# Performance work log

Hardware: AMD Instinct MI355X
Metric: run time of the kernel (lower is better)

Reference implementation:

```python
import jax, jax.numpy as jnp
import numpy as np

B, L, D, H, T = 4096, 7, 1024, 1024, 6


def setup_inputs() -> dict:
    key = jax.random.key(0)
    ks = jax.random.split(key, 20)
    s = 0.02
    inp = {
        "encoder_output": jax.random.normal(ks[0], (B, L, D), jnp.float32),
        "xes": jax.random.randint(ks[1], (B, T, 3), 0, L, jnp.int32),
        "idx": jax.random.randint(ks[2], (B,), 0, L, jnp.int32),
        "mask": jnp.ones((B, L), jnp.int32),
        # Attention params
        "Wq": jax.random.normal(ks[3], (H, H)) * s,
        "bq": jnp.zeros((H,)),
        "Wc": jax.random.normal(ks[4], (4, H, D)) * s,  # 4 context 1x1 convs stacked
        "bc": jnp.zeros((4, H)),
        "V4": jax.random.uniform(ks[5], (4, H), minval=-1.0, maxval=1.0),
        # Decoder params
        "Wi": jax.random.normal(ks[6], (H, D)) * s,  # index_linear
        "bi": jnp.zeros((H,)),
        "Wh": jax.random.normal(ks[7], (H, D)) * s,   # linear_h (no bias)
        "Wv": jax.random.normal(ks[8], (H, D)) * s,   # linear_v
        "Wsh": jax.random.normal(ks[9], (H, D)) * s,  # linears_h
        "Wsv": jax.random.normal(ks[10], (H, D)) * s, # linears_v
        "We": jax.random.normal(ks[11], (H, H)) * s,  # linear_edge
    }
    return inp


def _gather_rows(enc, i):
    # enc: [B, L, D], i: [B] -> enc[b, i[b], :]  == diagonal(index_select) in torch
    return jnp.take_along_axis(enc, i[:, None, None], axis=1)[:, 0]


def reference(encoder_output, xes, idx, mask, Wq, bq, Wc, bc, V4, Wi, bi, Wh, Wv, Wsh, Wsv, We):
    enc = encoder_output

    # --- recurrent subtree/edge accumulation over T steps (lax.scan) ---
    def step(carry, x):
        el, st = carry
        h_i, v_i, t = x  # each [B]
        h = _gather_rows(enc, h_i)  # [B, D]
        v = _gather_rows(enc, v_i)
        edge = jnp.where((t == 0)[:, None],
                         h @ Wh.T + v @ Wv.T,
                         v @ Wsv.T + h @ Wsh.T)          # [B, H]
        subtree = jnp.maximum(st, edge @ We.T)
        qt = jax.nn.relu(el + st)  # uses previous el/st, as in torch step()
        return (edge, subtree), qt

    z = jnp.zeros((B, H), enc.dtype)
    xs = (xes[:, :, 0].T, xes[:, :, 1].T, xes[:, :, 2].T)  # [T, B] each
    _, qts = jax.lax.scan(step, (z, z), xs)
    qt = qts[-1]  # last step's qt

    # --- query construction (index_linear applied and added twice, as in source) ---
    enc_idx = _gather_rows(enc, idx)           # [B, D]
    lin_idx = enc_idx @ Wi.T + bi              # [B, H]
    query = jax.nn.relu(qt + lin_idx)
    query = jax.nn.relu(query + lin_idx)

    # --- 4-way tanh attention ---
    inp = query @ Wq.T + bq                    # same input_linear for all 4 heads
    ctx = jnp.einsum('bld,khd->kbhl', enc, Wc) + bc[:, None, :, None]  # [4,B,H,L]
    att = jnp.einsum('kh,kbhl->bkl', V4, jnp.tanh(inp[None, :, :, None] + ctx))
    att = att.reshape(B, 4 * L)                # cat order: k-major, matches torch

    mask4 = jnp.tile(mask, (1, 4))
    att = jnp.where(mask4 != 0, att, -jnp.inf)
    att = 10.0 * jnp.tanh(att)
    alpha = jax.nn.softmax(att, axis=0)        # Softmax(dim=0) over batch, as in source

    # multinomial(ans, 1): per-row categorical (row-normalized), deterministic key
    skey = jax.random.key(42)
    indices = jax.random.categorical(skey, jnp.log(alpha), axis=1)[:, None]  # [B,1]
    p = jnp.take_along_axis(alpha, indices, axis=1)                           # [B,1]

    one_hot = (jnp.arange(L)[None, :] == indices).astype(mask.dtype)          # [B,L]
    mask_out = mask - one_hot
    return indices, p, mask_out
```

## Files before the change

kernel.cpp:

```cpp
#include <hip/hip_runtime.h>

#define NB 4096
#define NL 7
#define ND 1024
#define NH 1024
#define NT 6
#define NSTEP 5
#define GAP 0.02f
#define MAXF 1024

typedef __attribute__((ext_vector_type(8))) short bf16x8;
typedef __attribute__((ext_vector_type(4))) float f32x4;

__device__ __forceinline__ unsigned rotl32(unsigned x, int r) {
  return (x << r) | (x >> (32 - r));
}

__device__ __forceinline__ void threefry2x32(unsigned k0, unsigned k1,
                                             unsigned x0, unsigned x1,
                                             unsigned& o0, unsigned& o1) {
  unsigned ks2 = k0 ^ k1 ^ 0x1BD11BDAu;
#define TFR(R) { x0 += x1; x1 = rotl32(x1, (R)); x1 ^= x0; }
  x0 += k0; x1 += k1;
  TFR(13) TFR(15) TFR(26) TFR(6)
  x0 += k1; x1 += ks2 + 1u;
  TFR(17) TFR(29) TFR(16) TFR(24)
  x0 += ks2; x1 += k0 + 2u;
  TFR(13) TFR(15) TFR(26) TFR(6)
  x0 += k0; x1 += k1 + 3u;
  TFR(17) TFR(29) TFR(16) TFR(24)
  x0 += k1; x1 += ks2 + 4u;
  TFR(13) TFR(15) TFR(26) TFR(6)
  x0 += ks2; x1 += k0 + 5u;
#undef TFR
  o0 = x0; o1 = x1;
}

__device__ __forceinline__ float gumbel_for(int b, int j) {
  unsigned o0, o1;
  threefry2x32(0u, 42u, 0u, (unsigned)(b * 28 + j), o0, o1);
  unsigned bits = o0 ^ o1;
  const float TINY = 1.17549435e-38f;
  float u = __uint_as_float((bits >> 9) | 0x3f800000u) - 1.0f;
  u = fmaxf(TINY, u + TINY);
  return -logf(-logf(u));
}

__device__ __forceinline__ unsigned short f2bf(float f) {
  unsigned u = __float_as_uint(f);
  unsigned r = u + 0x7FFFu + ((u >> 16) & 1u);
  return (unsigned short)(r >> 16);
}
__device__ __forceinline__ float bf2f(unsigned short h) {
  return __uint_as_float(((unsigned)h) << 16);
}

__global__ __launch_bounds__(256) void k_split(
    const float* __restrict__ x, unsigned short* __restrict__ hi,
    unsigned short* __restrict__ lo) {
  const size_t i = ((size_t)blockIdx.x * 256 + threadIdx.x) * 4;
  float4 v = *(const float4*)(x + i);
  ushort4 h, l;
  h.x = f2bf(v.x); l.x = f2bf(v.x - bf2f(h.x));
  h.y = f2bf(v.y); l.y = f2bf(v.y - bf2f(h.y));
  h.z = f2bf(v.z); l.z = f2bf(v.z - bf2f(h.z));
  h.w = f2bf(v.w); l.w = f2bf(v.w - bf2f(h.w));
  *(ushort4*)(hi + i) = h;
  *(ushort4*)(lo + i) = l;
}

__device__ __forceinline__ void tile_compute(const float (*As)[68],
                                             const float (*Bs)[68],
                                             float acc[4][4], int tx, int ty) {
#pragma unroll
  for (int kk = 0; kk < 16; ++kk) {
    float4 a  = *(const float4*)&As[kk][ty * 4];
    float4 bb = *(const float4*)&Bs[kk][tx * 4];
    acc[0][0] += a.x * bb.x; acc[0][1] += a.x * bb.y; acc[0][2] += a.x * bb.z; acc[0][3] += a.x * bb.w;
    acc[1][0] += a.y * bb.x; acc[1][1] += a.y * bb.y; acc[1][2] += a.y * bb.z; acc[1][3] += a.y * bb.w;
    acc[2][0] += a.z * bb.x; acc[2][1] += a.z * bb.y; acc[2][2] += a.z * bb.z; acc[2][3] += a.z * bb.w;
    acc[3][0] += a.w * bb.x; acc[3][1] += a.w * bb.y; acc[3][2] += a.w * bb.z; acc[3][3] += a.w * bb.w;
  }
}

#define TILE_DECLS \
  __shared__ float As[16][68]; \
  __shared__ float Bs[16][68]; \
  float acc[4][4] = {}; \
  const int tid = threadIdx.x; \
  const int tx = tid & 15, ty = tid >> 4; \
  const int row0 = blockIdx.y * 64, col0 = blockIdx.x * 64; \
  const int lm = tid >> 2; \
  const int lk4 = (tid & 3) * 4;

#define STORE_AS(av) { As[lk4+0][lm]=(av).x; As[lk4+1][lm]=(av).y; As[lk4+2][lm]=(av).z; As[lk4+3][lm]=(av).w; }
#define STORE_BS(bv) { Bs[lk4+0][lm]=(bv).x; Bs[lk4+1][lm]=(bv).y; Bs[lk4+2][lm]=(bv).z; Bs[lk4+3][lm]=(bv).w; }

__global__ __launch_bounds__(256) void gemm_bias(
    const float* __restrict__ A, const int* __restrict__ gidx,
    const float* __restrict__ enc, const float* __restrict__ Bw,
    const float* __restrict__ bias, float* __restrict__ C) {
  TILE_DECLS
  const int r = row0 + lm;
  const float* arow = gidx ? (enc + (((size_t)r * NL + gidx[r]) << 10))
                           : (A + ((size_t)r << 10));
  const float* brow = Bw + ((size_t)(col0 + lm) << 10);
  for (int k0 = 0; k0 < ND; k0 += 16) {
    float4 av = *(const float4*)(arow + k0 + lk4);
    STORE_AS(av)
    float4 bv = *(const float4*)(brow + k0 + lk4);
    STORE_BS(bv)
    __syncthreads();
    tile_compute(As, Bs, acc, tx, ty);
    __syncthreads();
  }
#pragma unroll
  for (int i = 0; i < 4; ++i) {
    const int rr = row0 + ty * 4 + i;
    const int n0 = col0 + tx * 4;
    float4 v = make_float4(acc[i][0] + bias[n0 + 0], acc[i][1] + bias[n0 + 1],
                           acc[i][2] + bias[n0 + 2], acc[i][3] + bias[n0 + 3]);
    *(float4*)(C + ((size_t)rr << 10) + n0) = v;
  }
}

__global__ __launch_bounds__(256) void k_classify(
    const int* __restrict__ xes, int* __restrict__ cls_cnt,
    int* __restrict__ l0, int* __restrict__ l1) {
  const int r = blockIdx.x * 256 + threadIdx.x;
  if (r >= NSTEP * NB) return;
  const int b = r & (NB - 1), t = r >> 12;
  const int tt = xes[(b * NT + t) * 3 + 2];
  if (tt == 0) { int p = atomicAdd(&cls_cnt[0], 1); l0[p] = r; }
  else         { int p = atomicAdd(&cls_cnt[1], 1); l1[p] = r; }
}

__global__ __launch_bounds__(256) void g1_mfma(
    const int* __restrict__ cls_cnt, const int* __restrict__ l0,
    const int* __restrict__ l1, const int* __restrict__ xes,
    const unsigned short* __restrict__ enc_hi, const unsigned short* __restrict__ enc_lo,
    const unsigned short* __restrict__ w4hi, const unsigned short* __restrict__ w4lo,
    unsigned* __restrict__ ehilo, float* __restrict__ edge4) {
  const int n0c = cls_cnt[0], n1c = cls_cnt[1];
  const int tiles0 = (n0c + 127) >> 7, tiles1 = (n1c + 127) >> 7;
  const int bx = blockIdx.x;
  if (bx >= tiles0 + tiles1) return;
  int cls, mtile, nc;
  const int* list;
  if (bx < tiles0) { cls = 0; mtile = bx; nc = n0c; list = l0; }
  else { cls = 1; mtile = bx - tiles0; nc = n1c; list = l1; }

  __shared__ unsigned short sAhi[4096], sAlo[4096], sBhi[4096], sBlo[4096];
  const int tid = threadIdx.x;
  const int ncol0 = blockIdx.y * 128;

  const int ri = tid & 127;
  const int c0 = tid >> 7;
  const int c1 = c0 + 2;
  const int li = mtile * 128 + ri;
  const int rsrc = list[(li < nc) ? li : (nc - 1)];
  const int b = rsrc & (NB - 1), t = rsrc >> 12;
  const int hidx = xes[(b * NT + t) * 3 + 0];
  const int vidx = xes[(b * NT + t) * 3 + 1];
  const unsigned short* ha = enc_hi + (((size_t)b * NL + hidx) << 10);
  const unsigned short* la = enc_lo + (((size_t)b * NL + hidx) << 10);
  const unsigned short* hb = enc_hi + (((size_t)b * NL + vidx) << 10);
  const unsigned short* lb = enc_lo + (((size_t)b * NL + vidx) << 10);
  const size_t wrow = ((size_t)(ncol0 + ri)) << 10;

  const int wave = tid >> 6, lane = tid & 63;
  const int wm = wave >> 1, wn = wave & 1;
  const int q = lane >> 4, m16 = lane & 15;

  f32x4 acc[4][4] = {};

  for (int kt = 0; kt < 64; ++kt) {
    const int seg = (kt < 32) ? (cls * 2) : (cls * 2 + 1);
    const int kl = (kt & 31) * 32;
    const unsigned short* ah = (kt < 32) ? ha : hb;
    const unsigned short* al = (kt < 32) ? la : lb;
    bf16x8 vah0 = *(const bf16x8*)(ah + kl + c0 * 8);
    bf16x8 vah1 = *(const bf16x8*)(ah + kl + c1 * 8);
    bf16x8 val0 = *(const bf16x8*)(al + kl + c0 * 8);
    bf16x8 val1 = *(const bf16x8*)(al + kl + c1 * 8);
    const unsigned short* wh = w4hi + (((size_t)seg) << 20) + wrow + kl;
    const unsigned short* wl = w4lo + (((size_t)seg) << 20) + wrow + kl;
    bf16x8 vbh0 = *(const bf16x8*)(wh + c0 * 8);
    bf16x8 vbh1 = *(const bf16x8*)(wh + c1 * 8);
    bf16x8 vbl0 = *(const bf16x8*)(wl + c0 * 8);
    bf16x8 vbl1 = *(const bf16x8*)(wl + c1 * 8);
    *(bf16x8*)&sAhi[(c0 * 128 + ri) * 8] = vah0;
    *(bf16x8*)&sAhi[(c1 * 128 + ri) * 8] = vah1;
    *(bf16x8*)&sAlo[(c0 * 128 + ri) * 8] = val0;
    *(bf16x8*)&sAlo[(c1 * 128 + ri) * 8] = val1;
    *(bf16x8*)&sBhi[(c0 * 128 + ri) * 8] = vbh0;
    *(bf16x8*)&sBhi[(c1 * 128 + ri) * 8] = vbh1;
    *(bf16x8*)&sBlo[(c0 * 128 + ri) * 8] = vbl0;
    *(bf16x8*)&sBlo[(c1 * 128 + ri) * 8] = vbl1;
    __syncthreads();

    bf16x8 bh[4], bl[4];
#pragma unroll
    for (int tn = 0; tn < 4; ++tn) {
      const int nl = wn * 64 + tn * 16 + m16;
      bh[tn] = *(const bf16x8*)&sBhi[(q * 128 + nl) * 8];
      bl[tn] = *(const bf16x8*)&sBlo[(q * 128 + nl) * 8];
    }
#pragma unroll
    for (int tm = 0; tm < 4; ++tm) {
      const int ml = wm * 64 + tm * 16 + m16;
      bf16x8 ah8 = *(const bf16x8*)&sAhi[(q * 128 + ml) * 8];
      bf16x8 al8 = *(const bf16x8*)&sAlo[(q * 128 + ml) * 8];
#pragma unroll
      for (int tn = 0; tn < 4; ++tn) {
        acc[tm][tn] = __builtin_amdgcn_mfma_f32_16x16x32_bf16(ah8, bh[tn], acc[tm][tn], 0, 0, 0);
        acc[tm][tn] = __builtin_amdgcn_mfma_f32_16x16x32_bf16(al8, bh[tn], acc[tm][tn], 0, 0, 0);
        acc[tm][tn] = __builtin_amdgcn_mfma_f32_16x16x32_bf16(ah8, bl[tn], acc[tm][tn], 0, 0, 0);
      }
    }
    __syncthreads();
  }

#pragma unroll
  for (int tm = 0; tm < 4; ++tm) {
#pragma unroll
    for (int j = 0; j < 4; ++j) {
      const int rl = wm * 64 + tm * 16 + q * 4 + j;
      const int li2 = mtile * 128 + rl;
      if (li2 < nc) {
        const int rr = list[li2];
#pragma unroll
        for (int tn = 0; tn < 4; ++tn) {
          const int n = ncol0 + wn * 64 + tn * 16 + m16;
          const float val = acc[tm][tn][j];
          unsigned short h = f2bf(val);
          unsigned short l = f2bf(val - bf2f(h));
          ehilo[(size_t)rr * NH + n] = (unsigned)h | ((unsigned)l << 16);
          if (rr >= 4 * NB) edge4[(size_t)(rr - 4 * NB) * NH + n] = val;
        }
      }
    }
  }
}

__global__ __launch_bounds__(256) void g2_mfma(
    const unsigned* __restrict__ ehilo,
    const unsigned short* __restrict__ wehi, const unsigned short* __restrict__ welo,
    unsigned* __restrict__ st) {
  __shared__ unsigned short sAhi[4096], sAlo[4096], sBhi[4096], sBlo[4096];
  const int tid = threadIdx.x;
  const int row0 = blockIdx.x * 128;
  const int ncol0 = blockIdx.y * 128;

  const int ri = tid & 127;
  const int c0 = tid >> 7;
  const int c1 = c0 + 2;
  const size_t arow = (size_t)(row0 + ri) * NH;
  const size_t wrow = ((size_t)(ncol0 + ri)) << 10;

  const int wave = tid >> 6, lane = tid & 63;
  const int wm = wave >> 1, wn = wave & 1;
  const int q = lane >> 4, m16 = lane & 15;

  f32x4 acc[4][4] = {};

  for (int kt = 0; kt < 32; ++kt) {
    const int kl = kt * 32;
    uint4 p00 = *(const uint4*)(ehilo + arow + kl + c0 * 8);
    uint4 p01 = *(const uint4*)(ehilo + arow + kl + c0 * 8 + 4);
    uint4 p10 = *(const uint4*)(ehilo + arow + kl + c1 * 8);
    uint4 p11 = *(const uint4*)(ehilo + arow + kl + c1 * 8 + 4);
    bf16x8 ah0, al0, ah1, al1;
    {
      unsigned u[8] = {p00.x, p00.y, p00.z, p00.w, p01.x, p01.y, p01.z, p01.w};
#pragma unroll
      for (int i = 0; i < 8; ++i) { ah0[i] = (short)(u[i] & 0xffff); al0[i] = (short)(u[i] >> 16); }
      unsigned v[8] = {p10.x, p10.y, p10.z, p10.w, p11.x, p11.y, p11.z, p11.w};
#pragma unroll
      for (int i = 0; i < 8; ++i) { ah1[i] = (short)(v[i] & 0xffff); al1[i] = (short)(v[i] >> 16); }
    }
    bf16x8 vbh0 = *(const bf16x8*)(wehi + wrow + kl + c0 * 8);
    bf16x8 vbh1 = *(const bf16x8*)(wehi + wrow + kl + c1 * 8);
    bf16x8 vbl0 = *(const bf16x8*)(welo + wrow + kl + c0 * 8);
    bf16x8 vbl1 = *(const bf16x8*)(welo + wrow + kl + c1 * 8);
    *(bf16x8*)&sAhi[(c0 * 128 + ri) * 8] = ah0;
    *(bf16x8*)&sAhi[(c1 * 128 + ri) * 8] = ah1;
    *(bf16x8*)&sAlo[(c0 * 128 + ri) * 8] = al0;
    *(bf16x8*)&sAlo[(c1 * 128 + ri) * 8] = al1;
    *(bf16x8*)&sBhi[(c0 * 128 + ri) * 8] = vbh0;
    *(bf16x8*)&sBhi[(c1 * 128 + ri) * 8] = vbh1;
    *(bf16x8*)&sBlo[(c0 * 128 + ri) * 8] = vbl0;
    *(bf16x8*)&sBlo[(c1 * 128 + ri) * 8] = vbl1;
    __syncthreads();

    bf16x8 bh[4], bl[4];
#pragma unroll
    for (int tn = 0; tn < 4; ++tn) {
      const int nl = wn * 64 + tn * 16 + m16;
      bh[tn] = *(const bf16x8*)&sBhi[(q * 128 + nl) * 8];
      bl[tn] = *(const bf16x8*)&sBlo[(q * 128 + nl) * 8];
    }
#pragma unroll
    for (int tm = 0; tm < 4; ++tm) {
      const int ml = wm * 64 + tm * 16 + m16;
      bf16x8 ah8 = *(const bf16x8*)&sAhi[(q * 128 + ml) * 8];
      bf16x8 al8 = *(const bf16x8*)&sAlo[(q * 128 + ml) * 8];
#pragma unroll
      for (int tn = 0; tn < 4; ++tn) {
        acc[tm][tn] = __builtin_amdgcn_mfma_f32_16x16x32_bf16(ah8, bh[tn], acc[tm][tn], 0, 0, 0);
        acc[tm][tn] = __builtin_amdgcn_mfma_f32_16x16x32_bf16(al8, bh[tn], acc[tm][tn], 0, 0, 0);
        acc[tm][tn] = __builtin_amdgcn_mfma_f32_16x16x32_bf16(ah8, bl[tn], acc[tm][tn], 0, 0, 0);
      }
    }
    __syncthreads();
  }

#pragma unroll
  for (int tm = 0; tm < 4; ++tm) {
#pragma unroll
    for (int j = 0; j < 4; ++j) {
      const int rr = row0 + wm * 64 + tm * 16 + q * 4 + j;
      const int b = rr & (NB - 1);
#pragma unroll
      for (int tn = 0; tn < 4; ++tn) {
        const int n = ncol0 + wn * 64 + tn * 16 + m16;
        unsigned val = __float_as_uint(fmaxf(acc[tm][tn][j], 0.f));
        atomicMax(&st[(size_t)b * NH + n], val);
      }
    }
  }
}

__global__ __launch_bounds__(256) void g5_mfma(
    const unsigned short* __restrict__ Ahi, const unsigned short* __restrict__ Alo,
    const unsigned short* __restrict__ Bhi, const unsigned short* __restrict__ Blo,
    const float* __restrict__ inp, const float* __restrict__ bc,
    const float* __restrict__ V4, float* __restrict__ att) {
  __shared__ unsigned short sAhi[4096], sAlo[4096], sBhi[4096], sBlo[4096];
  __shared__ float red[128][32];

  const int tid = threadIdx.x;
  const int row0 = blockIdx.x * 128;
  const int ncol0 = blockIdx.y * 128;

  const int s0 = tid, s1 = tid + 256;
  const int c0 = s0 >> 7, r0 = s0 & 127;
  const int c1 = s1 >> 7, r1 = s1 & 127;
  size_t aoff0 = (size_t)(row0 + r0) * ND + c0 * 8;
  size_t aoff1 = (size_t)(row0 + r1) * ND + c1 * 8;
  size_t boff0 = (size_t)(ncol0 + r0) * ND + c0 * 8;
  size_t boff1 = (size_t)(ncol0 + r1) * ND + c1 * 8;

  const int wave = tid >> 6, lane = tid & 63;
  const int wm = wave >> 1, wn = wave & 1;
  const int q = lane >> 4, m16 = lane & 15;

  f32x4 acc[4][4] = {};

  for (int kt = 0; kt < 32; ++kt) {
    bf16x8 vah0 = *(const bf16x8*)(Ahi + aoff0);
    bf16x8 vah1 = *(const bf16x8*)(Ahi + aoff1);
    bf16x8 val0 = *(const bf16x8*)(Alo + aoff0);
    bf16x8 val1 = *(const bf16x8*)(Alo + aoff1);
    bf16x8 vbh0 = *(const bf16x8*)(Bhi + boff0);
    bf16x8 vbh1 = *(const bf16x8*)(Bhi + boff1);
    bf16x8 vbl0 = *(const bf16x8*)(Blo + boff0);
    bf16x8 vbl1 = *(const bf16x8*)(Blo + boff1);
    *(bf16x8*)&sAhi[s0 * 8] = vah0;
    *(bf16x8*)&sAhi[s1 * 8] = vah1;
    *(bf16x8*)&sAlo[s0 * 8] = val0;
    *(bf16x8*)&sAlo[s1 * 8] = val1;
    *(bf16x8*)&sBhi[s0 * 8] = vbh0;
    *(bf16x8*)&sBhi[s1 * 8] = vbh1;
    *(bf16x8*)&sBlo[s0 * 8] = vbl0;
    *(bf16x8*)&sBlo[s1 * 8] = vbl1;
    __syncthreads();

    bf16x8 bh[4], bl[4];
#pragma unroll
    for (int tn = 0; tn < 4; ++tn) {
      const int nl = wn * 64 + tn * 16 + m16;
      bh[tn] = *(const bf16x8*)&sBhi[(q * 128 + nl) * 8];
      bl[tn] = *(const bf16x8*)&sBlo[(q * 128 + nl) * 8];
    }
#pragma unroll
    for (int tm = 0; tm < 4; ++tm) {
      const int ml = wm * 64 + tm * 16 + m16;
      bf16x8 ah = *(const bf16x8*)&sAhi[(q * 128 + ml) * 8];
      bf16x8 al = *(const bf16x8*)&sAlo[(q * 128 + ml) * 8];
#pragma unroll
      for (int tn = 0; tn < 4; ++tn) {
        acc[tm][tn] = __builtin_amdgcn_mfma_f32_16x16x32_bf16(ah, bh[tn], acc[tm][tn], 0, 0, 0);
        acc[tm][tn] = __builtin_amdgcn_mfma_f32_16x16x32_bf16(al, bh[tn], acc[tm][tn], 0, 0, 0);
        acc[tm][tn] = __builtin_amdgcn_mfma_f32_16x16x32_bf16(ah, bl[tn], acc[tm][tn], 0, 0, 0);
      }
    }
    __syncthreads();
    aoff0 += 32; aoff1 += 32; boff0 += 32; boff1 += 32;
  }

  const int kq = ncol0 >> 10;
  float rowsum[16];
#pragma unroll
  for (int i = 0; i < 16; ++i) rowsum[i] = 0.f;
#pragma unroll
  for (int tm = 0; tm < 4; ++tm) {
#pragma unroll
    for (int tn = 0; tn < 4; ++tn) {
      const int n = ncol0 + wn * 64 + tn * 16 + m16;
      const int h = n & (NH - 1);
      const float v4 = V4[kq * NH + h];
      const float bcv = bc[kq * NH + h];
#pragma unroll
      for (int j = 0; j < 4; ++j) {
        const int R = row0 + wm * 64 + tm * 16 + q * 4 + j;
        const int b = R / NL;
        float val = acc[tm][tn][j] + inp[(size_t)b * NH + h] + bcv;
        rowsum[tm * 4 + j] += v4 * tanhf(val);
      }
    }
  }
#pragma unroll
  for (int tm = 0; tm < 4; ++tm)
#pragma unroll
    for (int j = 0; j < 4; ++j)
      red[wm * 64 + tm * 16 + q * 4 + j][wn * 16 + m16] = rowsum[tm * 4 + j];
  __syncthreads();
  if (tid < 128) {
    float ssum = 0.f;
#pragma unroll
    for (int x = 0; x < 32; ++x) ssum += red[tid][x];
    const int R = row0 + tid;
    const int b = R / NL, l = R - b * NL;
    atomicAdd(&att[b * 28 + kq * NL + l], ssum);
  }
}

__global__ __launch_bounds__(256) void k_query(
    const float* __restrict__ edge4, const float* __restrict__ st,
    const float* __restrict__ lin, float* __restrict__ query) {
  const size_t i = (size_t)blockIdx.x * 256 + threadIdx.x;
  float e4 = edge4[i];
  float qt = fmaxf(e4 + st[i], 0.f);
  float l = lin[i];
  float q = fmaxf(qt + l, 0.f);
  q = fmaxf(q + l, 0.f);
  query[i] = q;
}

__global__ __launch_bounds__(256) void k_finish(
    float* __restrict__ att, const int* __restrict__ mask) {
  const int i = blockIdx.x * 256 + threadIdx.x;
  const int b = i / 28;
  const int j = i - b * 28;
  const int l = j % NL;
  float v = att[i];
  att[i] = (mask[b * NL + l] != 0) ? (10.f * tanhf(v)) : -10.f;
}

__global__ __launch_bounds__(256) void k_colstats(
    const float* __restrict__ att, float* __restrict__ Mv, float* __restrict__ Sv) {
  const int j = blockIdx.x;
  const int tid = threadIdx.x;
  __shared__ float sm[256];
  float m = -INFINITY;
  for (int b = tid; b < NB; b += 256) m = fmaxf(m, att[b * 28 + j]);
  sm[tid] = m;
  __syncthreads();
  for (int s = 128; s > 0; s >>= 1) {
    if (tid < s) sm[tid] = fmaxf(sm[tid], sm[tid + s]);
    __syncthreads();
  }
  const float M = sm[0];
  __syncthreads();
  float sum = 0.f;
  for (int b = tid; b < NB; b += 256) sum += expf(att[b * 28 + j] - M);
  sm[tid] = sum;
  __syncthreads();
  for (int s = 128; s > 0; s >>= 1) {
    if (tid < s) sm[tid] += sm[tid + s];
    __syncthreads();
  }
  if (tid == 0) { Mv[j] = M; Sv[j] = sm[0]; }
}

__global__ __launch_bounds__(256) void k_sample(
    const float* __restrict__ att, const float* __restrict__ Mv,
    const float* __restrict__ Sv, const int* __restrict__ mask,
    float* __restrict__ out, int* __restrict__ flag,
    int* __restrict__ cnt, int* __restrict__ list) {
  const int b = blockIdx.x * 256 + threadIdx.x;
  if (b >= NB) return;
  float best = -INFINITY, second = -INFINITY;
  int bj = 0;
  for (int j = 0; j < 28; ++j) {
    float y = (att[b * 28 + j] - Mv[j]) - logf(Sv[j]) + gumbel_for(b, j);
    if (y > best) { second = best; best = y; bj = j; }
    else if (y > second) second = y;
  }
  out[b] = (float)bj;
  out[NB + b] = expf(att[b * 28 + bj] - Mv[bj]) / Sv[bj];
  const int* mrow = mask + b * NL;
#pragma unroll
  for (int l = 0; l < NL; ++l)
    out[2 * NB + (size_t)b * NL + l] = (float)(mrow[l] - ((l == bj) ? 1 : 0));
  const int f = (best - second < GAP) ? 1 : 0;
  flag[b] = f;
  if (f) {
    int pos = atomicAdd(cnt, 1);
    if (pos < MAXF) list[pos] = b;
  }
}

__global__ __launch_bounds__(256) void k_build_fl(
    const int* __restrict__ cnt, const int* __restrict__ list,
    const int* __restrict__ xes, int* __restrict__ fl_cnt,
    int* __restrict__ fl0, int* __restrict__ fl1) {
  const int it = blockIdx.x * 256 + threadIdx.x;
  const int n = (cnt[0] < MAXF) ? cnt[0] : MAXF;
  if (it >= n) return;
  const int b = list[it];
#pragma unroll
  for (int t = 0; t < NSTEP; ++t) {
    const int tt = xes[(b * NT + t) * 3 + 2];
    const int e = it * 8 + t;
    if (tt == 0) { int p = atomicAdd(&fl_cnt[0], 1); fl0[p] = e; }
    else         { int p = atomicAdd(&fl_cnt[1], 1); fl1[p] = e; }
  }
}

__global__ __launch_bounds__(256) void k_fix_edge(
    const int* __restrict__ fl_cnt, const int* __restrict__ fl0,
    const int* __restrict__ fl1, const int* __restrict__ list,
    const int* __restrict__ xes, const float* __restrict__ enc,
    const float* __restrict__ Wh, const float* __restrict__ Wv,
    const float* __restrict__ Wsh, const float* __restrict__ Wsv,
    float* __restrict__ edgeF) {
  const int n0c = fl_cnt[0], n1c = fl_cnt[1];
  const int tiles0 = (n0c + 63) >> 6, tiles1 = (n1c + 63) >> 6;
  const int bx = blockIdx.x;
  if (bx >= tiles0 + tiles1) return;
  int cls, mtile, nc;
  const int* fl;
  if (bx < tiles0) { cls = 0; mtile = bx; nc = n0c; fl = fl0; }
  else { cls = 1; mtile = bx - tiles0; nc = n1c; fl = fl1; }

  __shared__ float As[16][68];
  __shared__ float Bs[16][68];
  float acc[4][4] = {};
  const int tid = threadIdx.x;
  const int tx = tid & 15, ty = tid >> 4;
  const int col0 = blockIdx.y * 64;
  const int lm = tid >> 2;
  const int lk4 = (tid & 3) * 4;

  const int li = mtile * 64 + lm;
  const int e = fl[(li < nc) ? li : (nc - 1)];
  const int it = e >> 3, t = e & 7;
  const int b = list[it];
  const int hidx = xes[(b * NT + t) * 3 + 0];
  const int vidx = xes[(b * NT + t) * 3 + 1];
  const float* arow0 = enc + (((size_t)b * NL + hidx) << 10);
  const float* arow1 = enc + (((size_t)b * NL + vidx) << 10);
  const float* W0 = (cls == 0) ? Wh : Wsh;
  const float* W1 = (cls == 0) ? Wv : Wsv;
  const float* brow0 = W0 + ((size_t)(col0 + lm) << 10);
  const float* brow1 = W1 + ((size_t)(col0 + lm) << 10);

  for (int half = 0; half < 2; ++half) {
    const float* ar = half ? arow1 : arow0;
    const float* br = half ? brow1 : brow0;
    for (int k0 = 0; k0 < ND; k0 += 16) {
      float4 av = *(const float4*)(ar + k0 + lk4);
      STORE_AS(av)
      float4 bv = *(const float4*)(br + k0 + lk4);
      STORE_BS(bv)
      __syncthreads();
      tile_compute(As, Bs, acc, tx, ty);
      __syncthreads();
    }
  }
#pragma unroll
  for (int i = 0; i < 4; ++i) {
    const int li2 = mtile * 64 + ty * 4 + i;
    if (li2 < nc) {
      const int e2 = fl[li2];
      const int it2 = e2 >> 3, t2 = e2 & 7;
      *(float4*)(edgeF + (((size_t)(it2 * 5 + t2)) << 10) + col0 + tx * 4) =
          make_float4(acc[i][0], acc[i][1], acc[i][2], acc[i][3]);
    }
  }
}

__global__ __launch_bounds__(256) void k_fix_st(
    const int* __restrict__ cnt, const float* __restrict__ edgeF,
    const float* __restrict__ We, unsigned* __restrict__ stF) {
  const int n = (cnt[0] < MAXF) ? cnt[0] : MAXF;
  const int M = n * 5;
  const int tiles = (M + 63) >> 6;
  if ((int)blockIdx.x >= tiles) return;
  __shared__ float As[16][68];
  __shared__ float Bs[16][68];
  float acc[4][4] = {};
  const int tid = threadIdx.x;
  const int tx = tid & 15, ty = tid >> 4;
  const int row0 = blockIdx.x * 64, col0 = blockIdx.y * 64;
  const int lm = tid >> 2;
  const int lk4 = (tid & 3) * 4;
  const int r = row0 + lm;
  const int rc = (r < M) ? r : (M - 1);
  const float* arow = edgeF + ((size_t)rc << 10);
  const float* brow = We + ((size_t)(col0 + lm) << 10);
  for (int k0 = 0; k0 < NH; k0 += 16) {
    float4 av = *(const float4*)(arow + k0 + lk4);
    STORE_AS(av)
    float4 bv = *(const float4*)(brow + k0 + lk4);
    STORE_BS(bv)
    __syncthreads();
    tile_compute(As, Bs, acc, tx, ty);
    __syncthreads();
  }
#pragma unroll
  for (int i = 0; i < 4; ++i) {
    const int rr = row0 + ty * 4 + i;
    if (rr < M) {
      const int it = rr / 5;
#pragma unroll
      for (int j = 0; j < 4; ++j) {
        unsigned val = __float_as_uint(fmaxf(acc[i][j], 0.f));
        atomicMax(&stF[(size_t)it * NH + col0 + tx * 4 + j], val);
      }
    }
  }
}

__global__ __launch_bounds__(256) void k_fix_query(
    const int* __restrict__ cnt, const int* __restrict__ list,
    const float* __restrict__ edgeF, const float* __restrict__ stF,
    const float* __restrict__ lin, float* __restrict__ qF) {
  const int i = blockIdx.x * 256 + threadIdx.x;
  const int it = i >> 10;
  const int n = (cnt[0] < MAXF) ? cnt[0] : MAXF;
  if (it >= n) return;
  const int nn = i & (NH - 1);
  const int b = list[it];
  float e4 = edgeF[(((size_t)(it * 5 + 4)) << 10) + nn];
  float stv = stF[(size_t)it * NH + nn];
  float qt = fmaxf(e4 + stv, 0.f);
  float lb = lin[(size_t)b * NH + nn];
  float qv = fmaxf(fmaxf(qt + lb, 0.f) + lb, 0.f);
  qF[(size_t)it * NH + nn] = qv;
}

__global__ __launch_bounds__(256) void k_fix_inp(
    const int* __restrict__ cnt, const int* __restrict__ list,
    const float* __restrict__ qF, const float* __restrict__ Wq,
    const float* __restrict__ bq, float* __restrict__ inp) {
  const int n = (cnt[0] < MAXF) ? cnt[0] : MAXF;
  const int tiles = (n + 63) >> 6;
  if ((int)blockIdx.x >= tiles) return;
  __shared__ float As[16][68];
  __shared__ float Bs[16][68];
  float acc[4][4] = {};
  const int tid = threadIdx.x;
  const int tx = tid & 15, ty = tid >> 4;
  const int row0 = blockIdx.x * 64, col0 = blockIdx.y * 64;
  const int lm = tid >> 2;
  const int lk4 = (tid & 3) * 4;
  const int r = row0 + lm;
  const int rc = (r < n) ? r : (n - 1);
  const float* arow = qF + ((size_t)rc << 10);
  const float* brow = Wq + ((size_t)(col0 + lm) << 10);
  for (int k0 = 0; k0 < NH; k0 += 16) {
    float4 av = *(const float4*)(arow + k0 + lk4);
    STORE_AS(av)
    float4 bv = *(const float4*)(brow + k0 + lk4);
    STORE_BS(bv)
    __syncthreads();
    tile_compute(As, Bs, acc, tx, ty);
    __syncthreads();
  }
#pragma unroll
  for (int i = 0; i < 4; ++i) {
    const int rr = row0 + ty * 4 + i;
    if (rr < n) {
      const int b = list[rr];
      const int n0 = col0 + tx * 4;
      float4 v = make_float4(acc[i][0] + bq[n0 + 0], acc[i][1] + bq[n0 + 1],
                             acc[i][2] + bq[n0 + 2], acc[i][3] + bq[n0 + 3]);
      *(float4*)(inp + ((size_t)b << 10) + n0) = v;
    }
  }
}

__global__ __launch_bounds__(256) void k_fixup_att(
    const int* __restrict__ cnt, const int* __restrict__ list,
    const float* __restrict__ enc, const float* __restrict__ Wc,
    const float* __restrict__ bc, const float* __restrict__ V4,
    const float* __restrict__ inp, const int* __restrict__ mask,
    float* __restrict__ att) {
  const int kq = blockIdx.x;
  const int tid = threadIdx.x;
  __shared__ float sEnc[NL][ND];
  __shared__ float sm[256];
  const int n = (cnt[0] < MAXF) ? cnt[0] : MAXF;
  for (int it = blockIdx.y; it < n; it += gridDim.y) {
    const int b = list[it];
    for (int i = tid; i < NL * 256; i += 256) {
      const int l = i >> 8, c = (i & 255) * 4;
      *(float4*)&sEnc[l][c] = *(const float4*)(enc + (((size_t)b * NL + l) << 10) + c);
    }
    __syncthreads();
    float accl[NL];
#pragma unroll
    for (int l = 0; l < NL; ++l) accl[l] = 0.f;
    for (int hp = 0; hp < 2; ++hp) {
      const int h0 = tid + hp * 512;
      const int h1 = h0 + 256;
      const float* w0 = Wc + (((size_t)kq * NH + h0) << 10);
      const float* w1 = Wc + (((size_t)kq * NH + h1) << 10);
      float d0[NL], d1[NL];
#pragma unroll
      for (int l = 0; l < NL; ++l) { d0[l] = 0.f; d1[l] = 0.f; }
      for (int k = 0; k < ND; k += 4) {
        float4 a = *(const float4*)(w0 + k);
        float4 c = *(const float4*)(w1 + k);
#pragma unroll
        for (int l = 0; l < NL; ++l) {
          float4 e = *(const float4*)&sEnc[l][k];
          d0[l] += a.x * e.x + a.y * e.y + a.z * e.z + a.w * e.w;
          d1[l] += c.x * e.x + c.y * e.y + c.z * e.z + c.w * e.w;
        }
      }
      const float i0 = inp[(size_t)b * NH + h0], i1 = inp[(size_t)b * NH + h1];
      const float b0 = bc[kq * NH + h0], b1 = bc[kq * NH + h1];
      const float v0 = V4[kq * NH + h0], v1 = V4[kq * NH + h1];
#pragma unroll
      for (int l = 0; l < NL; ++l)
        accl[l] += v0 * tanhf(d0[l] + i0 + b0) + v1 * tanhf(d1[l] + i1 + b1);
    }
    for (int l = 0; l < NL; ++l) {
      sm[tid] = accl[l];
      __syncthreads();
      for (int s = 128; s > 0; s >>= 1) {
        if (tid < s) sm[tid] += sm[tid + s];
        __syncthreads();
      }
      if (tid == 0) {
        float a = (mask[b * NL + l] != 0) ? (10.f * tanhf(sm[0])) : -10.f;
        att[b * 28 + kq * NL + l] = a;
      }
      __syncthreads();
    }
    __syncthreads();
  }
}

__global__ __launch_bounds__(256) void k_resample(
    const int* __restrict__ flag, const float* __restrict__ att,
    const float* __restrict__ Mv, const float* __restrict__ Sv,
    const int* __restrict__ mask, float* __restrict__ out) {
  const int b = blockIdx.x * 256 + threadIdx.x;
  if (b >= NB) return;
  if (!flag[b]) return;
  float best = -INFINITY;
  int bj = 0;
  for (int j = 0; j < 28; ++j) {
    float y = (att[b * 28 + j] - Mv[j]) - logf(Sv[j]) + gumbel_for(b, j);
    if (y > best) { best = y; bj = j; }
  }
  out[b] = (float)bj;
  out[NB + b] = expf(att[b * 28 + bj] - Mv[bj]) / Sv[bj];
  const int* mrow = mask + b * NL;
#pragma unroll
  for (int l = 0; l < NL; ++l)
    out[2 * NB + (size_t)b * NL + l] = (float)(mrow[l] - ((l == bj) ? 1 : 0));
}

extern "C" void kernel_launch(void* const* d_in, const int* in_sizes, int n_in,
                              void* d_out, int out_size, void* d_ws, size_t ws_size,
                              hipStream_t stream) {
  const float* enc  = (const float*)d_in[0];
  const int*   xes  = (const int*)d_in[1];
  const int*   idx  = (const int*)d_in[2];
  const int*   mask = (const int*)d_in[3];
  const float* Wq   = (const float*)d_in[4];
  const float* bq   = (const float*)d_in[5];
  const float* Wc   = (const float*)d_in[6];
  const float* bc   = (const float*)d_in[7];
  const float* V4   = (const float*)d_in[8];
  const float* Wi   = (const float*)d_in[9];
  const float* bi   = (const float*)d_in[10];
  const float* Wh   = (const float*)d_in[11];
  const float* Wv   = (const float*)d_in[12];
  const float* Wsh  = (const float*)d_in[13];
  const float* Wsv  = (const float*)d_in[14];
  const float* We   = (const float*)d_in[15];
  (void)in_sizes; (void)n_in; (void)out_size; (void)ws_size;

  char* p = (char*)d_ws;
  float* edge4 = (float*)p;                 p += (size_t)NB * NH * 4;
  unsigned* ehilo = (unsigned*)p;           p += (size_t)NSTEP * NB * NH * 4;
  float* st = (float*)p;                    p += (size_t)NB * NH * 4;
  float* lin = (float*)p;                   p += (size_t)NB * NH * 4;
  float* query = (float*)p;                 p += (size_t)NB * NH * 4;
  float* inp = (float*)p;                   p += (size_t)NB * NH * 4;
  float* att = (float*)p;                   p += (size_t)NB * 28 * 4;
  float* Mv = (float*)p;                    p += 28 * 4;
  float* Sv = (float*)p;                    p += 28 * 4;
  int* flag = (int*)p;                      p += NB * 4;
  int* cnt = (int*)p;                       p += 4 * 4;
  int* list = (int*)p;                      p += NB * 4;
  int* cls_cnt = (int*)p;                   p += 2 * 4;
  int* l0 = (int*)p;                        p += NSTEP * NB * 4;
  int* l1 = (int*)p;                        p += NSTEP * NB * 4;
  int* fl_cnt = (int*)p;                    p += 2 * 4;
  int* fl0 = (int*)p;                       p += NSTEP * MAXF * 4;
  int* fl1 = (int*)p;                       p += NSTEP * MAXF * 4;
  float* edgeF = (float*)p;                 p += (size_t)NSTEP * MAXF * NH * 4;
  float* stF = (float*)p;                   p += (size_t)MAXF * NH * 4;
  float* qF = (float*)p;                    p += (size_t)MAXF * NH * 4;
  unsigned short* enc_hi = (unsigned short*)p; p += (size_t)NB * NL * ND * 2;
  unsigned short* enc_lo = (unsigned short*)p; p += (size_t)NB * NL * ND * 2;
  unsigned short* w4hi = (unsigned short*)p;   p += (size_t)4 * NH * ND * 2;
  unsigned short* w4lo = (unsigned short*)p;   p += (size_t)4 * NH * ND * 2;
  unsigned short* wehi = (unsigned short*)p;   p += (size_t)NH * ND * 2;
  unsigned short* welo = (unsigned short*)p;   p += (size_t)NH * ND * 2;
  unsigned short* wc_hi = (unsigned short*)p;  p += (size_t)4 * NH * ND * 2;
  unsigned short* wc_lo = (unsigned short*)p;  p += (size_t)4 * NH * ND * 2;
  float* out = (float*)d_out;

  hipMemsetAsync(st, 0, (size_t)NB * NH * sizeof(float), stream);
  hipMemsetAsync(att, 0, (size_t)NB * 28 * sizeof(float), stream);
  hipMemsetAsync(cnt, 0, sizeof(int), stream);
  hipMemsetAsync(cls_cnt, 0, 2 * sizeof(int), stream);
  hipMemsetAsync(fl_cnt, 0, 2 * sizeof(int), stream);
  hipMemsetAsync(stF, 0, (size_t)MAXF * NH * sizeof(float), stream);

  dim3 blk(256);
  k_split<<<dim3((NB * NL * ND) / 1024), blk, 0, stream>>>(enc, enc_hi, enc_lo);
  k_split<<<dim3((4 * NH * ND) / 1024), blk, 0, stream>>>(Wc, wc_hi, wc_lo);
  k_split<<<dim3((NH * ND) / 1024), blk, 0, stream>>>(Wh, w4hi, w4lo);
  k_split<<<dim3((NH * ND) / 1024), blk, 0, stream>>>(Wv, w4hi + (size_t)NH * ND, w4lo + (size_t)NH * ND);
  k_split<<<dim3((NH * ND) / 1024), blk, 0, stream>>>(Wsh, w4hi + (size_t)2 * NH * ND, w4lo + (size_t)2 * NH * ND);
  k_split<<<dim3((NH * ND) / 1024), blk, 0, stream>>>(Wsv, w4hi + (size_t)3 * NH * ND, w4lo + (size_t)3 * NH * ND);
  k_split<<<dim3((NH * ND) / 1024), blk, 0, stream>>>(We, wehi, welo);
  k_classify<<<dim3((NSTEP * NB) / 256), blk, 0, stream>>>(xes, cls_cnt, l0, l1);
  g1_mfma<<<dim3(162, 8), blk, 0, stream>>>(cls_cnt, l0, l1, xes, enc_hi, enc_lo,
                                            w4hi, w4lo, ehilo, edge4);
  gemm_bias<<<dim3(16, 64), blk, 0, stream>>>(nullptr, idx, enc, Wi, bi, lin);
  g2_mfma<<<dim3(160, 8), blk, 0, stream>>>(ehilo, wehi, welo, (unsigned*)st);
  k_query<<<dim3((NB * NH) / 256), blk, 0, stream>>>(edge4, st, lin, query);
  gemm_bias<<<dim3(16, 64), blk, 0, stream>>>(query, nullptr, enc, Wq, bq, inp);
  g5_mfma<<<dim3(224, 32), blk, 0, stream>>>(enc_hi, enc_lo, wc_hi, wc_lo,
                                             inp, bc, V4, att);
  k_finish<<<dim3((NB * 28) / 256), blk, 0, stream>>>(att, mask);
  k_colstats<<<dim3(28), blk, 0, stream>>>(att, Mv, Sv);
  k_sample<<<dim3(NB / 256), blk, 0, stream>>>(att, Mv, Sv, mask, out, flag, cnt, list);
  k_build_fl<<<dim3(MAXF / 256), blk, 0, stream>>>(cnt, list, xes, fl_cnt, fl0, fl1);
  k_fix_edge<<<dim3(81, 16), blk, 0, stream>>>(fl_cnt, fl0, fl1, list, xes, enc,
                                               Wh, Wv, Wsh, Wsv, edgeF);
  k_fix_st<<<dim3(80, 16), blk, 0, stream>>>(cnt, edgeF, We, (unsigned*)stF);
  k_fix_query<<<dim3((MAXF * NH) / 256), blk, 0, stream>>>(cnt, list, edgeF, stF, lin, qF);
  k_fix_inp<<<dim3(16, 16), blk, 0, stream>>>(cnt, list, qF, Wq, bq, inp);
  k_fixup_att<<<dim3(4, 64), blk, 0, stream>>>(cnt, list, enc, Wc, bc, V4, inp, mask, att);
  k_resample<<<dim3(NB / 256), blk, 0, stream>>>(flag, att, Mv, Sv, mask, out);
}
```

Measured before the change: 3.442 ms.

## Replace fp32 SIMT GEMMs with split-bf16 MFMA and swap grid axes

The two fp32 tiled SIMT GEMMs (index_linear and input_linear) become a new MFMA kernel that uses a three-product hi/lo bf16 split, with Wi and Wq pre-split. k_query is vectorised and now writes query directly as hi/lo bf16, so the fp32 query buffer is gone. All MFMA kernels swap grid x/y so consecutive blocks share the same row tile across column tiles, which should improve L2 reuse of the A operand. g5 also overlays its reduction buffer on the staging shared memory to cut LDS use. The cost is two extra split kernels and approximate-fp32 accuracy in these GEMMs.

```diff
diff --git a/kernel.cpp b/kernel.cpp
--- a/kernel.cpp
+++ b/kernel.cpp
@@ -83,46 +83,8 @@
   }
 }
 
-#define TILE_DECLS \
-  __shared__ float As[16][68]; \
-  __shared__ float Bs[16][68]; \
-  float acc[4][4] = {}; \
-  const int tid = threadIdx.x; \
-  const int tx = tid & 15, ty = tid >> 4; \
-  const int row0 = blockIdx.y * 64, col0 = blockIdx.x * 64; \
-  const int lm = tid >> 2; \
-  const int lk4 = (tid & 3) * 4;
-
 #define STORE_AS(av) { As[lk4+0][lm]=(av).x; As[lk4+1][lm]=(av).y; As[lk4+2][lm]=(av).z; As[lk4+3][lm]=(av).w; }
 #define STORE_BS(bv) { Bs[lk4+0][lm]=(bv).x; Bs[lk4+1][lm]=(bv).y; Bs[lk4+2][lm]=(bv).z; Bs[lk4+3][lm]=(bv).w; }
-
-__global__ __launch_bounds__(256) void gemm_bias(
-    const float* __restrict__ A, const int* __restrict__ gidx,
-    const float* __restrict__ enc, const float* __restrict__ Bw,
-    const float* __restrict__ bias, float* __restrict__ C) {
-  TILE_DECLS
-  const int r = row0 + lm;
-  const float* arow = gidx ? (enc + (((size_t)r * NL + gidx[r]) << 10))
-                           : (A + ((size_t)r << 10));
-  const float* brow = Bw + ((size_t)(col0 + lm) << 10);
-  for (int k0 = 0; k0 < ND; k0 += 16) {
-    float4 av = *(const float4*)(arow + k0 + lk4);
-    STORE_AS(av)
-    float4 bv = *(const float4*)(brow + k0 + lk4);
-    STORE_BS(bv)
-    __syncthreads();
-    tile_compute(As, Bs, acc, tx, ty);
-    __syncthreads();
-  }
-#pragma unroll
-  for (int i = 0; i < 4; ++i) {
-    const int rr = row0 + ty * 4 + i;
-    const int n0 = col0 + tx * 4;
-    float4 v = make_float4(acc[i][0] + bias[n0 + 0], acc[i][1] + bias[n0 + 1],
-                           acc[i][2] + bias[n0 + 2], acc[i][3] + bias[n0 + 3]);
-    *(float4*)(C + ((size_t)rr << 10) + n0) = v;
-  }
-}
 
 __global__ __launch_bounds__(256) void k_classify(
     const int* __restrict__ xes, int* __restrict__ cls_cnt,
@@ -143,7 +105,7 @@
     unsigned* __restrict__ ehilo, float* __restrict__ edge4) {
   const int n0c = cls_cnt[0], n1c = cls_cnt[1];
   const int tiles0 = (n0c + 127) >> 7, tiles1 = (n1c + 127) >> 7;
-  const int bx = blockIdx.x;
+  const int bx = blockIdx.y;
   if (bx >= tiles0 + tiles1) return;
   int cls, mtile, nc;
   const int* list;
@@ -152,7 +114,7 @@
 
   __shared__ unsigned short sAhi[4096], sAlo[4096], sBhi[4096], sBlo[4096];
   const int tid = threadIdx.x;
-  const int ncol0 = blockIdx.y * 128;
+  const int ncol0 = blockIdx.x * 128;
 
   const int ri = tid & 127;
   const int c0 = tid >> 7;
@@ -249,8 +211,8 @@
     unsigned* __restrict__ st) {
   __shared__ unsigned short sAhi[4096], sAlo[4096], sBhi[4096], sBlo[4096];
   const int tid = threadIdx.x;
-  const int row0 = blockIdx.x * 128;
-  const int ncol0 = blockIdx.y * 128;
+  const int row0 = blockIdx.y * 128;
+  const int ncol0 = blockIdx.x * 128;
 
   const int ri = tid & 127;
   const int c0 = tid >> 7;
@@ -331,23 +293,27 @@
   }
 }
 
-__global__ __launch_bounds__(256) void g5_mfma(
+__global__ __launch_bounds__(256) void g_lin_mfma(
     const unsigned short* __restrict__ Ahi, const unsigned short* __restrict__ Alo,
+    const int* __restrict__ gidx,
     const unsigned short* __restrict__ Bhi, const unsigned short* __restrict__ Blo,
-    const float* __restrict__ inp, const float* __restrict__ bc,
-    const float* __restrict__ V4, float* __restrict__ att) {
-  __shared__ unsigned short sAhi[4096], sAlo[4096], sBhi[4096], sBlo[4096];
-  __shared__ float red[128][32];
-
+    const float* __restrict__ bias, float* __restrict__ C) {
+  __shared__ __align__(16) char smem[32768];
+  unsigned short* sAhi = (unsigned short*)smem;
+  unsigned short* sAlo = (unsigned short*)(smem + 8192);
+  unsigned short* sBhi = (unsigned short*)(smem + 16384);
+  unsigned short* sBlo = (unsigned short*)(smem + 24576);
   const int tid = threadIdx.x;
-  const int row0 = blockIdx.x * 128;
-  const int ncol0 = blockIdx.y * 128;
-
+  const int row0 = blockIdx.y * 128;
+  const int ncol0 = blockIdx.x * 128;
   const int s0 = tid, s1 = tid + 256;
   const int c0 = s0 >> 7, r0 = s0 & 127;
   const int c1 = s1 >> 7, r1 = s1 & 127;
-  size_t aoff0 = (size_t)(row0 + r0) * ND + c0 * 8;
-  size_t aoff1 = (size_t)(row0 + r1) * ND + c1 * 8;
+  const int ar0 = row0 + r0, ar1 = row0 + r1;
+  size_t abase0 = gidx ? (((size_t)(ar0 * NL + gidx[ar0])) << 10) : ((size_t)ar0 << 10);
+  size_t abase1 = gidx ? (((size_t)(ar1 * NL + gidx[ar1])) << 10) : ((size_t)ar1 << 10);
+  size_t aoff0 = abase0 + c0 * 8;
+  size_t aoff1 = abase1 + c1 * 8;
   size_t boff0 = (size_t)(ncol0 + r0) * ND + c0 * 8;
   size_t boff1 = (size_t)(ncol0 + r1) * ND + c1 * 8;
 
@@ -399,6 +365,92 @@
     aoff0 += 32; aoff1 += 32; boff0 += 32; boff1 += 32;
   }
 
+#pragma unroll
+  for (int tm = 0; tm < 4; ++tm) {
+#pragma unroll
+    for (int j = 0; j < 4; ++j) {
+      const int R = row0 + wm * 64 + tm * 16 + q * 4 + j;
+#pragma unroll
+      for (int tn = 0; tn < 4; ++tn) {
+        const int n = ncol0 + wn * 64 + tn * 16 + m16;
+        C[(size_t)R * NH + n] = acc[tm][tn][j] + bias[n];
+      }
+    }
+  }
+}
+
+__global__ __launch_bounds__(256) void g5_mfma(
+    const unsigned short* __restrict__ Ahi, const unsigned short* __restrict__ Alo,
+    const unsigned short* __restrict__ Bhi, const unsigned short* __restrict__ Blo,
+    const float* __restrict__ inp, const float* __restrict__ bc,
+    const float* __restrict__ V4, float* __restrict__ att) {
+  __shared__ __align__(16) char smem[32768];
+  unsigned short* sAhi = (unsigned short*)smem;
+  unsigned short* sAlo = (unsigned short*)(smem + 8192);
+  unsigned short* sBhi = (unsigned short*)(smem + 16384);
+  unsigned short* sBlo = (unsigned short*)(smem + 24576);
+  float (*red)[33] = (float(*)[33])smem;
+
+  const int tid = threadIdx.x;
+  const int row0 = blockIdx.y * 128;
+  const int ncol0 = blockIdx.x * 128;
+
+  const int s0 = tid, s1 = tid + 256;
+  const int c0 = s0 >> 7, r0 = s0 & 127;
+  const int c1 = s1 >> 7, r1 = s1 & 127;
+  size_t aoff0 = (size_t)(row0 + r0) * ND + c0 * 8;
+  size_t aoff1 = (size_t)(row0 + r1) * ND + c1 * 8;
+  size_t boff0 = (size_t)(ncol0 + r0) * ND + c0 * 8;
+  size_t boff1 = (size_t)(ncol0 + r1) * ND + c1 * 8;
+
+  const int wave = tid >> 6, lane = tid & 63;
+  const int wm = wave >> 1, wn = wave & 1;
+  const int q = lane >> 4, m16 = lane & 15;
+
+  f32x4 acc[4][4] = {};
+
+  for (int kt = 0; kt < 32; ++kt) {
+    bf16x8 vah0 = *(const bf16x8*)(Ahi + aoff0);
+    bf16x8 vah1 = *(const bf16x8*)(Ahi + aoff1);
+    bf16x8 val0 = *(const bf16x8*)(Alo + aoff0);
+    bf16x8 val1 = *(const bf16x8*)(Alo + aoff1);
+    bf16x8 vbh0 = *(const bf16x8*)(Bhi + boff0);
+    bf16x8 vbh1 = *(const bf16x8*)(Bhi + boff1);
+    bf16x8 vbl0 = *(const bf16x8*)(Blo + boff0);
+    bf16x8 vbl1 = *(const bf16x8*)(Blo + boff1);
+    *(bf16x8*)&sAhi[s0 * 8] = vah0;
+    *(bf16x8*)&sAhi[s1 * 8] = vah1;
+    *(bf16x8*)&sAlo[s0 * 8] = val0;
+    *(bf16x8*)&sAlo[s1 * 8] = val1;
+    *(bf16x8*)&sBhi[s0 * 8] = vbh0;
+    *(bf16x8*)&sBhi[s1 * 8] = vbh1;
+    *(bf16x8*)&sBlo[s0 * 8] = vbl0;
+    *(bf16x8*)&sBlo[s1 * 8] = vbl1;
+    __syncthreads();
+
+    bf16x8 bh[4], bl[4];
+#pragma unroll
+    for (int tn = 0; tn < 4; ++tn) {
+      const int nl = wn * 64 + tn * 16 + m16;
+      bh[tn] = *(const bf16x8*)&sBhi[(q * 128 + nl) * 8];
+      bl[tn] = *(const bf16x8*)&sBlo[(q * 128 + nl) * 8];
+    }
+#pragma unroll
+    for (int tm = 0; tm < 4; ++tm) {
+      const int ml = wm * 64 + tm * 16 + m16;
+      bf16x8 ah = *(const bf16x8*)&sAhi[(q * 128 + ml) * 8];
+      bf16x8 al = *(const bf16x8*)&sAlo[(q * 128 + ml) * 8];
+#pragma unroll
+      for (int tn = 0; tn < 4; ++tn) {
+        acc[tm][tn] = __builtin_amdgcn_mfma_f32_16x16x32_bf16(ah, bh[tn], acc[tm][tn], 0, 0, 0);
+        acc[tm][tn] = __builtin_amdgcn_mfma_f32_16x16x32_bf16(al, bh[tn], acc[tm][tn], 0, 0, 0);
+        acc[tm][tn] = __builtin_amdgcn_mfma_f32_16x16x32_bf16(ah, bl[tn], acc[tm][tn], 0, 0, 0);
+      }
+    }
+    __syncthreads();
+    aoff0 += 32; aoff1 += 32; boff0 += 32; boff1 += 32;
+  }
+
   const int kq = ncol0 >> 10;
   float rowsum[16];
 #pragma unroll
@@ -438,14 +490,24 @@
 
 __global__ __launch_bounds__(256) void k_query(
     const float* __restrict__ edge4, const float* __restrict__ st,
-    const float* __restrict__ lin, float* __restrict__ query) {
-  const size_t i = (size_t)blockIdx.x * 256 + threadIdx.x;
-  float e4 = edge4[i];
-  float qt = fmaxf(e4 + st[i], 0.f);
-  float l = lin[i];
-  float q = fmaxf(qt + l, 0.f);
-  q = fmaxf(q + l, 0.f);
-  query[i] = q;
+    const float* __restrict__ lin, unsigned short* __restrict__ qhi,
+    unsigned short* __restrict__ qlo) {
+  const size_t i = ((size_t)blockIdx.x * 256 + threadIdx.x) * 4;
+  float4 e4 = *(const float4*)(edge4 + i);
+  float4 sv = *(const float4*)(st + i);
+  float4 lv = *(const float4*)(lin + i);
+  float qv[4];
+  qv[0] = fmaxf(fmaxf(fmaxf(e4.x + sv.x, 0.f) + lv.x, 0.f) + lv.x, 0.f);
+  qv[1] = fmaxf(fmaxf(fmaxf(e4.y + sv.y, 0.f) + lv.y, 0.f) + lv.y, 0.f);
+  qv[2] = fmaxf(fmaxf(fmaxf(e4.z + sv.z, 0.f) + lv.z, 0.f) + lv.z, 0.f);
+  qv[3] = fmaxf(fmaxf(fmaxf(e4.w + sv.w, 0.f) + lv.w, 0.f) + lv.w, 0.f);
+  ushort4 h, l;
+  h.x = f2bf(qv[0]); l.x = f2bf(qv[0] - bf2f(h.x));
+  h.y = f2bf(qv[1]); l.y = f2bf(qv[1] - bf2f(h.y));
+  h.z = f2bf(qv[2]); l.z = f2bf(qv[2] - bf2f(h.z));
+  h.w = f2bf(qv[3]); l.w = f2bf(qv[3] - bf2f(h.w));
+  *(ushort4*)(qhi + i) = h;
+  *(ushort4*)(qlo + i) = l;
 }
 
 __global__ __launch_bounds__(256) void k_finish(
@@ -803,7 +865,6 @@
   unsigned* ehilo = (unsigned*)p;           p += (size_t)NSTEP * NB * NH * 4;
   float* st = (float*)p;                    p += (size_t)NB * NH * 4;
   float* lin = (float*)p;                   p += (size_t)NB * NH * 4;
-  float* query = (float*)p;                 p += (size_t)NB * NH * 4;
   float* inp = (float*)p;                   p += (size_t)NB * NH * 4;
   float* att = (float*)p;                   p += (size_t)NB * 28 * 4;
   float* Mv = (float*)p;                    p += 28 * 4;
@@ -828,6 +889,12 @@
   unsigned short* welo = (unsigned short*)p;   p += (size_t)NH * ND * 2;
   unsigned short* wc_hi = (unsigned short*)p;  p += (size_t)4 * NH * ND * 2;
   unsigned short* wc_lo = (unsigned short*)p;  p += (size_t)4 * NH * ND * 2;
+  unsigned short* wihi = (unsigned short*)p;   p += (size_t)NH * ND * 2;
+  unsigned short* wilo = (unsigned short*)p;   p += (size_t)NH * ND * 2;
+  unsigned short* wqhi = (unsigned short*)p;   p += (size_t)NH * ND * 2;
+  unsigned short* wqlo = (unsigned short*)p;   p += (size_t)NH * ND * 2;
+  unsigned short* qhi = (unsigned short*)p;    p += (size_t)NB * NH * 2;
+  unsigned short* qlo = (unsigned short*)p;    p += (size_t)NB * NH * 2;
   float* out = (float*)d_out;
 
   hipMemsetAsync(st, 0, (size_t)NB * NH * sizeof(float), stream);
@@ -845,14 +912,16 @@
   k_split<<<dim3((NH * ND) / 1024), blk, 0, stream>>>(Wsh, w4hi + (size_t)2 * NH * ND, w4lo + (size_t)2 * NH * ND);
   k_split<<<dim3((NH * ND) / 1024), blk, 0, stream>>>(Wsv, w4hi + (size_t)3 * NH * ND, w4lo + (size_t)3 * NH * ND);
   k_split<<<dim3((NH * ND) / 1024), blk, 0, stream>>>(We, wehi, welo);
+  k_split<<<dim3((NH * ND) / 1024), blk, 0, stream>>>(Wi, wihi, wilo);
+  k_split<<<dim3((NH * ND) / 1024), blk, 0, stream>>>(Wq, wqhi, wqlo);
   k_classify<<<dim3((NSTEP * NB) / 256), blk, 0, stream>>>(xes, cls_cnt, l0, l1);
-  g1_mfma<<<dim3(162, 8), blk, 0, stream>>>(cls_cnt, l0, l1, xes, enc_hi, enc_lo,
+  g1_mfma<<<dim3(8, 162), blk, 0, stream>>>(cls_cnt, l0, l1, xes, enc_hi, enc_lo,
                                             w4hi, w4lo, ehilo, edge4);
-  gemm_bias<<<dim3(16, 64), blk, 0, stream>>>(nullptr, idx, enc, Wi, bi, lin);
-  g2_mfma<<<dim3(160, 8), blk, 0, stream>>>(ehilo, wehi, welo, (unsigned*)st);
-  k_query<<<dim3((NB * NH) / 256), blk, 0, stream>>>(edge4, st, lin, query);
-  gemm_bias<<<dim3(16, 64), blk, 0, stream>>>(query, nullptr, enc, Wq, bq, inp);
-  g5_mfma<<<dim3(224, 32), blk, 0, stream>>>(enc_hi, enc_lo, wc_hi, wc_lo,
+  g_lin_mfma<<<dim3(8, 32), blk, 0, stream>>>(enc_hi, enc_lo, idx, wihi, wilo, bi, lin);
+  g2_mfma<<<dim3(8, 160), blk, 0, stream>>>(ehilo, wehi, welo, (unsigned*)st);
+  k_query<<<dim3((NB * NH) / 1024), blk, 0, stream>>>(edge4, st, lin, qhi, qlo);
+  g_lin_mfma<<<dim3(8, 32), blk, 0, stream>>>(qhi, qlo, nullptr, wqhi, wqlo, bq, inp);
+  g5_mfma<<<dim3(32, 224), blk, 0, stream>>>(enc_hi, enc_lo, wc_hi, wc_lo,
                                              inp, bc, V4, att);
   k_finish<<<dim3((NB * 28) / 256), blk, 0, stream>>>(att, mask);
   k_colstats<<<dim3(28), blk, 0, stream>>>(att, Mv, Sv);
```

New measurement: 3.236 ms. 1.06x faster.
